# Optimization experiments

Hardware: AMD Instinct MI355X
Metric: run time of the kernel (lower is better)

The kernel has to match this reference:

```python
import jax, jax.numpy as jnp
import numpy as np
import math

S, D = 8192, 128

def setup_inputs() -> dict:
    key = jax.random.key(0)
    kq, kk, kv = jax.random.split(key, 3)
    return {
        "q": jax.random.normal(kq, (S, D), dtype=jnp.float32),
        "k": jax.random.normal(kk, (S, D), dtype=jnp.float32),
        "v": jax.random.normal(kv, (S, D), dtype=jnp.float32),
    }

def reference(q, k, v):
    # scores: [S, S]; scale by sqrt(d) as in the torch module
    scale = 1.0 / math.sqrt(q.shape[1])
    scores = (q @ k.T) * scale
    attn = jax.nn.softmax(scores, axis=-1)
    return attn @ v
```

## Files before the change

kernel.cpp:

```cpp
#include <hip/hip_runtime.h>
#include <hip/hip_bf16.h>

#define SEQ 8192
#define HD 128
#define BM 128
#define BN 64
#define NQT (SEQ / BM)
#define THREADS 256
#define KTP 130
#define VTP 66

typedef __bf16 bf16_t;
typedef __bf16 bf16x2 __attribute__((ext_vector_type(2)));
typedef __bf16 bf16x8 __attribute__((ext_vector_type(8)));
typedef float f32x4 __attribute__((ext_vector_type(4)));
typedef float f32x16 __attribute__((ext_vector_type(16)));
typedef unsigned int u32x4 __attribute__((ext_vector_type(4)));

#if __has_builtin(__builtin_amdgcn_exp2f)
__device__ inline float exp2_fast(float x) { return __builtin_amdgcn_exp2f(x); }
#else
__device__ inline float exp2_fast(float x) { return exp2f(x); }
#endif

__global__ __launch_bounds__(256) void prep_kernel(const float* __restrict__ K,
                                                   const float* __restrict__ V,
                                                   bf16_t* __restrict__ Kb,
                                                   bf16_t* __restrict__ VT) {
  const int b = (int)blockIdx.x;
  const int tid = (int)threadIdx.x;
  if (b < 256) {
    __shared__ float tile[64][65];
    const int s0 = (b & 127) * 64;
    const int d0 = (b >> 7) * 64;
    const int r = tid >> 2;
    const int c0 = (tid & 3) * 16;
#pragma unroll
    for (int j4 = 0; j4 < 4; ++j4) {
      float4 x = *(const float4*)&V[(size_t)(s0 + r) * HD + d0 + c0 + j4 * 4];
      tile[r][c0 + j4 * 4 + 0] = x.x;
      tile[r][c0 + j4 * 4 + 1] = x.y;
      tile[r][c0 + j4 * 4 + 2] = x.z;
      tile[r][c0 + j4 * 4 + 3] = x.w;
    }
    __syncthreads();
    bf16x8 w0, w1;
#pragma unroll
    for (int j = 0; j < 8; ++j) w0[j] = (bf16_t)tile[c0 + j][r];
#pragma unroll
    for (int j = 0; j < 8; ++j) w1[j] = (bf16_t)tile[c0 + 8 + j][r];
    *(bf16x8*)&VT[(size_t)(d0 + r) * SEQ + s0 + c0] = w0;
    *(bf16x8*)&VT[(size_t)(d0 + r) * SEQ + s0 + c0 + 8] = w1;
  } else {
    const int base = (b - 256) * 2048 + tid * 8;
    float4 a = *(const float4*)&K[base];
    float4 c = *(const float4*)&K[base + 4];
    bf16x8 f;
    f[0] = (bf16_t)a.x; f[1] = (bf16_t)a.y; f[2] = (bf16_t)a.z; f[3] = (bf16_t)a.w;
    f[4] = (bf16_t)c.x; f[5] = (bf16_t)c.y; f[6] = (bf16_t)c.z; f[7] = (bf16_t)c.w;
    *(bf16x8*)&Kb[base] = f;
  }
}

__global__ __launch_bounds__(THREADS, 2) void fattn_kernel(
    const float* __restrict__ Q, const bf16_t* __restrict__ Kb,
    const bf16_t* __restrict__ VT, float* __restrict__ Opart,
    float* __restrict__ Lpart, int kshift, int nit) {
  __shared__ __align__(16) bf16_t kts[2][BN][KTP];
  __shared__ __align__(16) bf16_t vts[2][HD][VTP];

  const int tid = (int)threadIdx.x;
  const int lane = tid & 63;
  const int w = tid >> 6;
  const int h = lane >> 5;
  const int n32 = lane & 31;

  const int qt = (int)blockIdx.x >> kshift;
  const int sp = (int)blockIdx.x & ((1 << kshift) - 1);
  const int qbase = qt * BM;
  const int kbase0 = sp * (nit * BN);

  const float SC2 = 0.08838834764831845f * 1.4426950408889634f;

  const int kr0 = tid >> 4;
  const int kc8 = (tid & 15) * 8;
  const int vd0 = tid >> 3;
  const int vc8 = (tid & 7) * 8;

  bf16x8 qf[8];
  {
    const float* qp = Q + (size_t)(qbase + w * 32 + n32) * HD + h * 8;
#pragma unroll
    for (int kk = 0; kk < 8; ++kk) {
      float4 a = *(const float4*)(qp + kk * 16);
      float4 b = *(const float4*)(qp + kk * 16 + 4);
      bf16x8 f;
      f[0] = (bf16_t)(a.x * SC2); f[1] = (bf16_t)(a.y * SC2);
      f[2] = (bf16_t)(a.z * SC2); f[3] = (bf16_t)(a.w * SC2);
      f[4] = (bf16_t)(b.x * SC2); f[5] = (bf16_t)(b.y * SC2);
      f[6] = (bf16_t)(b.z * SC2); f[7] = (bf16_t)(b.w * SC2);
      qf[kk] = f;
    }
  }

  f32x16 o_acc[4];
#pragma unroll
  for (int i = 0; i < 4; ++i)
#pragma unroll
    for (int e = 0; e < 16; ++e) o_acc[i][e] = 0.f;
  float l_acc = 0.f;

  {
#pragma unroll
    for (int j = 0; j < 4; ++j) {
      bf16x8 kr = *(const bf16x8*)&Kb[(size_t)(kbase0 + kr0 + 16 * j) * HD + kc8];
      *(bf16x8*)&kts[0][kr0 + 16 * j][kc8] = kr;
    }
#pragma unroll
    for (int j = 0; j < 4; ++j) {
      bf16x8 vr = *(const bf16x8*)&VT[(size_t)(vd0 + 32 * j) * SEQ + kbase0 + vc8];
      *(bf16x8*)&vts[0][vd0 + 32 * j][vc8] = vr;
    }
  }
  __syncthreads();

  for (int it = 0; it < nit; ++it) {
    const int cur = it & 1;
    const int nxt = cur ^ 1;
    const int nk = (it + 1 < nit) ? kbase0 + (it + 1) * BN : kbase0;
    bf16x8 kreg[4], vreg[4];
#pragma unroll
    for (int j = 0; j < 4; ++j)
      kreg[j] = *(const bf16x8*)&Kb[(size_t)(nk + kr0 + 16 * j) * HD + kc8];
#pragma unroll
    for (int j = 0; j < 4; ++j)
      vreg[j] = *(const bf16x8*)&VT[(size_t)(vd0 + 32 * j) * SEQ + nk + vc8];

    f32x16 sacc[2];
#pragma unroll
    for (int nt = 0; nt < 2; ++nt)
#pragma unroll
      for (int e = 0; e < 16; ++e) sacc[nt][e] = 0.f;
#pragma unroll
    for (int kk = 0; kk < 8; ++kk) {
#pragma unroll
      for (int nt = 0; nt < 2; ++nt) {
        bf16x8 af = *(const bf16x8*)&kts[cur][nt * 32 + n32][kk * 16 + h * 8];
        sacc[nt] = __builtin_amdgcn_mfma_f32_32x32x16_bf16(af, qf[kk], sacc[nt], 0, 0, 0);
      }
    }

#pragma unroll
    for (int nt = 0; nt < 2; ++nt) {
      float pf[16];
#pragma unroll
      for (int r = 0; r < 16; ++r) pf[r] = exp2_fast(sacc[nt][r]);
#pragma unroll
      for (int r = 0; r < 16; ++r) l_acc += pf[r];
      unsigned int pk[8];
#pragma unroll
      for (int g = 0; g < 4; ++g) {
        bf16x2 p0; p0[0] = (bf16_t)pf[4 * g + 0]; p0[1] = (bf16_t)pf[4 * g + 1];
        bf16x2 p1; p1[0] = (bf16_t)pf[4 * g + 2]; p1[1] = (bf16_t)pf[4 * g + 3];
        pk[2 * g + 0] = __builtin_bit_cast(unsigned int, p0);
        pk[2 * g + 1] = __builtin_bit_cast(unsigned int, p1);
      }
#pragma unroll
      for (int kk2 = 0; kk2 < 2; ++kk2) {
        const unsigned int sA = pk[4 * kk2 + 0], sB = pk[4 * kk2 + 1];
        const unsigned int sC = pk[4 * kk2 + 2], sD = pk[4 * kk2 + 3];
        unsigned int s0 = h ? sA : sC, s1 = h ? sB : sD;
        unsigned int r0 = __shfl_xor(s0, 32);
        unsigned int r1 = __shfl_xor(s1, 32);
        unsigned int o0 = h ? sC : sA, o1 = h ? sD : sB;
        u32x4 fv;
        fv[0] = h ? r0 : o0; fv[1] = h ? r1 : o1;
        fv[2] = h ? o0 : r0; fv[3] = h ? o1 : r1;
        bf16x8 pa = __builtin_bit_cast(bf16x8, fv);
#pragma unroll
        for (int ot = 0; ot < 4; ++ot) {
          bf16x8 vb = *(const bf16x8*)&vts[cur][ot * 32 + n32][nt * 32 + kk2 * 16 + h * 8];
          o_acc[ot] = __builtin_amdgcn_mfma_f32_32x32x16_bf16(pa, vb, o_acc[ot], 0, 0, 0);
        }
      }
    }

#pragma unroll
    for (int j = 0; j < 4; ++j) *(bf16x8*)&kts[nxt][kr0 + 16 * j][kc8] = kreg[j];
#pragma unroll
    for (int j = 0; j < 4; ++j) *(bf16x8*)&vts[nxt][vd0 + 32 * j][vc8] = vreg[j];
    __syncthreads();
  }

  {
    float* op = Opart + ((size_t)sp * SEQ + qbase + w * 32) * HD;
#pragma unroll
    for (int ot = 0; ot < 4; ++ot)
#pragma unroll
      for (int reg = 0; reg < 16; ++reg) {
        const int row = (reg & 3) + 8 * (reg >> 2) + 4 * h;
        op[row * HD + ot * 32 + n32] = o_acc[ot][reg];
      }
    float l = l_acc + __shfl_xor(l_acc, 32);
    if (lane < 32)
      Lpart[(size_t)sp * SEQ + qbase + w * 32 + n32] = l;
  }
}

__global__ __launch_bounds__(256) void combine_kernel(const float* __restrict__ Opart,
                                                      const float* __restrict__ Lpart,
                                                      float* __restrict__ out, int ksplit) {
  const int tid = (int)threadIdx.x;
  const int row = (int)blockIdx.x * 8 + (tid >> 5);
  const int c0 = (tid & 31) * 4;
  float lsum = 0.f;
  for (int s = 0; s < ksplit; ++s) lsum += Lpart[(size_t)s * SEQ + row];
  f32x4 acc;
#pragma unroll
  for (int e = 0; e < 4; ++e) acc[e] = 0.f;
  for (int s = 0; s < ksplit; ++s) {
    f32x4 o = *(const f32x4*)&Opart[((size_t)s * SEQ + row) * HD + c0];
#pragma unroll
    for (int e = 0; e < 4; ++e) acc[e] += o[e];
  }
  const float inv = 1.0f / lsum;
  f32x4 res;
#pragma unroll
  for (int e = 0; e < 4; ++e) res[e] = acc[e] * inv;
  *(f32x4*)&out[(size_t)row * HD + c0] = res;
}

extern "C" void kernel_launch(void* const* d_in, const int* in_sizes, int n_in,
                              void* d_out, int out_size, void* d_ws, size_t ws_size,
                              hipStream_t stream) {
  const float* Q = (const float*)d_in[0];
  const float* K = (const float*)d_in[1];
  const float* V = (const float*)d_in[2];
  float* out = (float*)d_out;

  int ksplit = 8, kshift = 3;
  while (ksplit > 1) {
    size_t need = (size_t)ksplit * SEQ * HD * 4
                + (size_t)ksplit * SEQ * 4
                + (size_t)SEQ * HD * 2 * 2;
    if (need <= ws_size) break;
    ksplit >>= 1; kshift--;
  }

  char* ws = (char*)d_ws;
  float* Opart = (float*)ws;
  float* Lpart = (float*)(ws + (size_t)ksplit * SEQ * HD * 4);
  bf16_t* Kb = (bf16_t*)(ws + (size_t)ksplit * SEQ * HD * 4 + (size_t)ksplit * SEQ * 4);
  bf16_t* VT = Kb + (size_t)SEQ * HD;

  const int nit = SEQ / (ksplit * BN);

  prep_kernel<<<768, 256, 0, stream>>>(K, V, Kb, VT);
  fattn_kernel<<<NQT * ksplit, THREADS, 0, stream>>>(Q, Kb, VT, Opart, Lpart, kshift, nit);
  combine_kernel<<<SEQ / 8, 256, 0, stream>>>(Opart, Lpart, out, ksplit);
}
```

Measured before the change: 121.8 us.

## Split each key tile across two wave groups with an LDS reduction

The block grows to 512 threads (8 waves). Two wave groups each process half of every 64-key tile for the same 128 query rows, which halves per-wave work per iteration and the per-thread K/V staging loads. At the end, group 1 writes its partial O and l to shared memory and group 0 adds them before storing, which costs an extra barrier and LDS traffic. The launch bound is also raised to 4 blocks per CU. That caps the register budget per wave, while the ~67KB LDS per block likely prevents that occupancy from being reached, so register spilling is a risk.

After: 224.5 us. 84.2% more time.

```diff
diff --git a/kernel.cpp b/kernel.cpp
--- a/kernel.cpp
+++ b/kernel.cpp
@@ -6,9 +6,11 @@
 #define BM 128
 #define BN 64
 #define NQT (SEQ / BM)
-#define THREADS 256
+#define THREADS 512
 #define KTP 130
 #define VTP 66
+#define KT_BYTES (2 * BN * KTP * 2)
+#define SMEM_BYTES (KT_BYTES + 2 * HD * VTP * 2)
 
 typedef __bf16 bf16_t;
 typedef __bf16 bf16x2 __attribute__((ext_vector_type(2)));
@@ -62,16 +64,19 @@
   }
 }
 
-__global__ __launch_bounds__(THREADS, 2) void fattn_kernel(
+__global__ __launch_bounds__(THREADS, 4) void fattn_kernel(
     const float* __restrict__ Q, const bf16_t* __restrict__ Kb,
     const bf16_t* __restrict__ VT, float* __restrict__ Opart,
     float* __restrict__ Lpart, int kshift, int nit) {
-  __shared__ __align__(16) bf16_t kts[2][BN][KTP];
-  __shared__ __align__(16) bf16_t vts[2][HD][VTP];
+  __shared__ __align__(16) char smem[SMEM_BYTES];
+  bf16_t (*kts)[BN][KTP] = (bf16_t(*)[BN][KTP])smem;
+  bf16_t (*vts)[HD][VTP] = (bf16_t(*)[HD][VTP])(smem + KT_BYTES);
 
   const int tid = (int)threadIdx.x;
   const int lane = tid & 63;
   const int w = tid >> 6;
+  const int qw = w & 3;
+  const int g = w >> 2;
   const int h = lane >> 5;
   const int n32 = lane & 31;
 
@@ -89,7 +94,7 @@
 
   bf16x8 qf[8];
   {
-    const float* qp = Q + (size_t)(qbase + w * 32 + n32) * HD + h * 8;
+    const float* qp = Q + (size_t)(qbase + qw * 32 + n32) * HD + h * 8;
 #pragma unroll
     for (int kk = 0; kk < 8; ++kk) {
       float4 a = *(const float4*)(qp + kk * 16);
@@ -112,14 +117,14 @@
 
   {
 #pragma unroll
-    for (int j = 0; j < 4; ++j) {
-      bf16x8 kr = *(const bf16x8*)&Kb[(size_t)(kbase0 + kr0 + 16 * j) * HD + kc8];
-      *(bf16x8*)&kts[0][kr0 + 16 * j][kc8] = kr;
-    }
-#pragma unroll
-    for (int j = 0; j < 4; ++j) {
-      bf16x8 vr = *(const bf16x8*)&VT[(size_t)(vd0 + 32 * j) * SEQ + kbase0 + vc8];
-      *(bf16x8*)&vts[0][vd0 + 32 * j][vc8] = vr;
+    for (int j = 0; j < 2; ++j) {
+      bf16x8 kr = *(const bf16x8*)&Kb[(size_t)(kbase0 + kr0 + 32 * j) * HD + kc8];
+      *(bf16x8*)&kts[0][kr0 + 32 * j][kc8] = kr;
+    }
+#pragma unroll
+    for (int j = 0; j < 2; ++j) {
+      bf16x8 vr = *(const bf16x8*)&VT[(size_t)(vd0 + 64 * j) * SEQ + kbase0 + vc8];
+      *(bf16x8*)&vts[0][vd0 + 64 * j][vc8] = vr;
     }
   }
   __syncthreads();
@@ -128,82 +133,89 @@
     const int cur = it & 1;
     const int nxt = cur ^ 1;
     const int nk = (it + 1 < nit) ? kbase0 + (it + 1) * BN : kbase0;
-    bf16x8 kreg[4], vreg[4];
-#pragma unroll
-    for (int j = 0; j < 4; ++j)
-      kreg[j] = *(const bf16x8*)&Kb[(size_t)(nk + kr0 + 16 * j) * HD + kc8];
-#pragma unroll
-    for (int j = 0; j < 4; ++j)
-      vreg[j] = *(const bf16x8*)&VT[(size_t)(vd0 + 32 * j) * SEQ + nk + vc8];
-
-    f32x16 sacc[2];
-#pragma unroll
-    for (int nt = 0; nt < 2; ++nt)
-#pragma unroll
-      for (int e = 0; e < 16; ++e) sacc[nt][e] = 0.f;
+    bf16x8 kreg[2], vreg[2];
+#pragma unroll
+    for (int j = 0; j < 2; ++j)
+      kreg[j] = *(const bf16x8*)&Kb[(size_t)(nk + kr0 + 32 * j) * HD + kc8];
+#pragma unroll
+    for (int j = 0; j < 2; ++j)
+      vreg[j] = *(const bf16x8*)&VT[(size_t)(vd0 + 64 * j) * SEQ + nk + vc8];
+
+    f32x16 sacc;
+#pragma unroll
+    for (int e = 0; e < 16; ++e) sacc[e] = 0.f;
 #pragma unroll
     for (int kk = 0; kk < 8; ++kk) {
-#pragma unroll
-      for (int nt = 0; nt < 2; ++nt) {
-        bf16x8 af = *(const bf16x8*)&kts[cur][nt * 32 + n32][kk * 16 + h * 8];
-        sacc[nt] = __builtin_amdgcn_mfma_f32_32x32x16_bf16(af, qf[kk], sacc[nt], 0, 0, 0);
+      bf16x8 af = *(const bf16x8*)&kts[cur][g * 32 + n32][kk * 16 + h * 8];
+      sacc = __builtin_amdgcn_mfma_f32_32x32x16_bf16(af, qf[kk], sacc, 0, 0, 0);
+    }
+
+    float pf[16];
+#pragma unroll
+    for (int r = 0; r < 16; ++r) pf[r] = exp2_fast(sacc[r]);
+#pragma unroll
+    for (int r = 0; r < 16; ++r) l_acc += pf[r];
+    unsigned int pk[8];
+#pragma unroll
+    for (int gg = 0; gg < 4; ++gg) {
+      bf16x2 p0; p0[0] = (bf16_t)pf[4 * gg + 0]; p0[1] = (bf16_t)pf[4 * gg + 1];
+      bf16x2 p1; p1[0] = (bf16_t)pf[4 * gg + 2]; p1[1] = (bf16_t)pf[4 * gg + 3];
+      pk[2 * gg + 0] = __builtin_bit_cast(unsigned int, p0);
+      pk[2 * gg + 1] = __builtin_bit_cast(unsigned int, p1);
+    }
+#pragma unroll
+    for (int kk2 = 0; kk2 < 2; ++kk2) {
+      const unsigned int sA = pk[4 * kk2 + 0], sB = pk[4 * kk2 + 1];
+      const unsigned int sC = pk[4 * kk2 + 2], sD = pk[4 * kk2 + 3];
+      unsigned int s0 = h ? sA : sC, s1 = h ? sB : sD;
+      unsigned int r0 = __shfl_xor(s0, 32);
+      unsigned int r1 = __shfl_xor(s1, 32);
+      unsigned int o0 = h ? sC : sA, o1 = h ? sD : sB;
+      u32x4 fv;
+      fv[0] = h ? r0 : o0; fv[1] = h ? r1 : o1;
+      fv[2] = h ? o0 : r0; fv[3] = h ? o1 : r1;
+      bf16x8 pa = __builtin_bit_cast(bf16x8, fv);
+#pragma unroll
+      for (int ot = 0; ot < 4; ++ot) {
+        bf16x8 vb = *(const bf16x8*)&vts[cur][ot * 32 + n32][g * 32 + kk2 * 16 + h * 8];
+        o_acc[ot] = __builtin_amdgcn_mfma_f32_32x32x16_bf16(pa, vb, o_acc[ot], 0, 0, 0);
       }
     }
 
 #pragma unroll
-    for (int nt = 0; nt < 2; ++nt) {
-      float pf[16];
-#pragma unroll
-      for (int r = 0; r < 16; ++r) pf[r] = exp2_fast(sacc[nt][r]);
-#pragma unroll
-      for (int r = 0; r < 16; ++r) l_acc += pf[r];
-      unsigned int pk[8];
-#pragma unroll
-      for (int g = 0; g < 4; ++g) {
-        bf16x2 p0; p0[0] = (bf16_t)pf[4 * g + 0]; p0[1] = (bf16_t)pf[4 * g + 1];
-        bf16x2 p1; p1[0] = (bf16_t)pf[4 * g + 2]; p1[1] = (bf16_t)pf[4 * g + 3];
-        pk[2 * g + 0] = __builtin_bit_cast(unsigned int, p0);
-        pk[2 * g + 1] = __builtin_bit_cast(unsigned int, p1);
-      }
-#pragma unroll
-      for (int kk2 = 0; kk2 < 2; ++kk2) {
-        const unsigned int sA = pk[4 * kk2 + 0], sB = pk[4 * kk2 + 1];
-        const unsigned int sC = pk[4 * kk2 + 2], sD = pk[4 * kk2 + 3];
-        unsigned int s0 = h ? sA : sC, s1 = h ? sB : sD;
-        unsigned int r0 = __shfl_xor(s0, 32);
-        unsigned int r1 = __shfl_xor(s1, 32);
-        unsigned int o0 = h ? sC : sA, o1 = h ? sD : sB;
-        u32x4 fv;
-        fv[0] = h ? r0 : o0; fv[1] = h ? r1 : o1;
-        fv[2] = h ? o0 : r0; fv[3] = h ? o1 : r1;
-        bf16x8 pa = __builtin_bit_cast(bf16x8, fv);
-#pragma unroll
-        for (int ot = 0; ot < 4; ++ot) {
-          bf16x8 vb = *(const bf16x8*)&vts[cur][ot * 32 + n32][nt * 32 + kk2 * 16 + h * 8];
-          o_acc[ot] = __builtin_amdgcn_mfma_f32_32x32x16_bf16(pa, vb, o_acc[ot], 0, 0, 0);
-        }
-      }
-    }
-
-#pragma unroll
-    for (int j = 0; j < 4; ++j) *(bf16x8*)&kts[nxt][kr0 + 16 * j][kc8] = kreg[j];
-#pragma unroll
-    for (int j = 0; j < 4; ++j) *(bf16x8*)&vts[nxt][vd0 + 32 * j][vc8] = vreg[j];
+    for (int j = 0; j < 2; ++j) *(bf16x8*)&kts[nxt][kr0 + 32 * j][kc8] = kreg[j];
+#pragma unroll
+    for (int j = 0; j < 2; ++j) *(bf16x8*)&vts[nxt][vd0 + 64 * j][vc8] = vreg[j];
     __syncthreads();
   }
 
-  {
-    float* op = Opart + ((size_t)sp * SEQ + qbase + w * 32) * HD;
+  float* osum = (float*)smem;
+  float* lsum = (float*)(smem + 65536);
+  if (g == 1) {
 #pragma unroll
     for (int ot = 0; ot < 4; ++ot)
 #pragma unroll
       for (int reg = 0; reg < 16; ++reg) {
         const int row = (reg & 3) + 8 * (reg >> 2) + 4 * h;
-        op[row * HD + ot * 32 + n32] = o_acc[ot][reg];
+        osum[(qw * 32 + row) * HD + ot * 32 + n32] = o_acc[ot][reg];
+      }
+    float l = l_acc + __shfl_xor(l_acc, 32);
+    if (lane < 32) lsum[qw * 32 + n32] = l;
+  }
+  __syncthreads();
+  if (g == 0) {
+    float* op = Opart + ((size_t)sp * SEQ + qbase + qw * 32) * HD;
+#pragma unroll
+    for (int ot = 0; ot < 4; ++ot)
+#pragma unroll
+      for (int reg = 0; reg < 16; ++reg) {
+        const int row = (reg & 3) + 8 * (reg >> 2) + 4 * h;
+        op[row * HD + ot * 32 + n32] =
+            o_acc[ot][reg] + osum[(qw * 32 + row) * HD + ot * 32 + n32];
       }
     float l = l_acc + __shfl_xor(l_acc, 32);
     if (lane < 32)
-      Lpart[(size_t)sp * SEQ + qbase + w * 32 + n32] = l;
+      Lpart[(size_t)sp * SEQ + qbase + qw * 32 + n32] = l + lsum[qw * 32 + n32];
   }
 }
 
```
